# Kernel tuning notes

Measured on AMD Instinct MI355X. Metric: run time of the kernel, lower is better.

Reference implementation:

```python
import jax, jax.numpy as jnp
import numpy as np

EPS = 1e-5
INF = 1e5


def setup_inputs() -> dict:
    key = jax.random.key(0)
    ks = iter(jax.random.split(key, 32))
    B, N, F, H, NH, C = 2, 384, 64, 64, 4, 32
    def lin(k, fi, fo):
        return jax.random.normal(k, (fi, fo), jnp.float32) / np.sqrt(fi).astype(np.float32)
    d = {}
    d['h'] = jax.random.normal(next(ks), (B, N, F), jnp.float32)
    d['x'] = jax.random.normal(next(ks), (B, N, 3), jnp.float32)
    # edge_model (ConcatenationFilter): Linear(2F+1,H), SiLU, Linear(H,H), SiLU
    d['We0'] = lin(next(ks), 2 * F + 1, H); d['be0'] = jnp.zeros(H, jnp.float32)
    d['We1'] = lin(next(ks), H, H);         d['be1'] = jnp.zeros(H, jnp.float32)
    # semantic_attention_mlp: Linear(H, n_heads), LeakyReLU(0.2)
    d['Ws'] = lin(next(ks), H, NH);         d['bs'] = jnp.zeros(NH, jnp.float32)
    # coefficients_mlp: Linear(H,H), SiLU, Linear(H,C)
    d['Wc0'] = lin(next(ks), H, H);         d['bc0'] = jnp.zeros(H, jnp.float32)
    d['Wc1'] = lin(next(ks), H, C);         d['bc1'] = jnp.zeros(C, jnp.float32)
    # post_norm_mlp: Linear(C,H), SiLU, Linear(H,H)
    d['Wp0'] = lin(next(ks), C, H);         d['bp0'] = jnp.zeros(H, jnp.float32)
    d['Wp1'] = lin(next(ks), H, H);         d['bp1'] = jnp.zeros(H, jnp.float32)
    # coordinate_mlp: Linear(H,H), SiLU, Linear(H,1,bias=False) init gain 1e-3
    d['Wx0'] = lin(next(ks), H, H);         d['bx0'] = jnp.zeros(H, jnp.float32)
    d['Wx1'] = lin(next(ks), H, 1) * 1e-3
    # node_mlp: Linear(NH*H + H + F, H), SiLU, Linear(H, F)
    d['Wn0'] = lin(next(ks), NH * H + H + F, H); d['bn0'] = jnp.zeros(H, jnp.float32)
    d['Wn1'] = lin(next(ks), H, F);         d['bn1'] = jnp.zeros(F, jnp.float32)
    d['log_gamma'] = jnp.zeros(NH, jnp.float32)
    return d


def _forward(h, x, We0, be0, We1, be1, Ws, bs, Wc0, bc0, Wc1, bc1,
             Wp0, bp0, Wp1, bp1, Wx0, bx0, Wx1, Wn0, bn0, Wn1, bn1, log_gamma):
    B, N, F = h.shape
    silu = jax.nn.silu

    # pairwise displacements and distances: (B,N,N,3), (B,N,N,1)
    x_minus_xt = x[:, :, None, :] - x[:, None, :, :]
    norm = jnp.sqrt(jnp.sum(x_minus_xt * x_minus_xt, axis=-1, keepdims=True) + EPS)

    # pairwise node-feature concat + distance -> edge MLP (ConcatenationFilter)
    hi = jnp.broadcast_to(h[:, :, None, :], (B, N, N, F))
    hj = jnp.broadcast_to(h[:, None, :, :], (B, N, N, F))
    e_in = jnp.concatenate([hi, hj, norm], axis=-1)           # (B,N,N,2F+1)
    h_e = silu(silu(e_in @ We0 + be0) @ We1 + be1)            # (B,N,N,H)

    eye = jnp.eye(N, dtype=h.dtype)[None, :, :, None]         # mask self-edges

    # euclidean attention per head, softmax over neighbors j (axis=-2)
    eu = jax.nn.softmax(-(norm + INF * eye) * jnp.exp(log_gamma), axis=-2)  # (B,N,N,NH)
    # semantic attention
    sem_logits = jax.nn.leaky_relu(h_e @ Ws + bs, 0.2) - INF * eye
    sem = jax.nn.softmax(sem_logits, axis=-2)                 # (B,N,N,NH)
    comb = eu * sem
    comb = comb / (jnp.sum(comb, axis=-2, keepdims=True) + EPS)

    # attention-weighted multi-head edge features, aggregated over neighbors
    h_e_att = (comb[..., :, None] * h_e[..., None, :]).reshape(B, N, N, -1)  # (B,N,N,NH*H)
    h_e_agg = jnp.sum(h_e_att, axis=-2)                       # (B,N,NH*H)

    # spatial attention: equivariant combinations of unit direction vectors
    coeff = silu(h_e @ Wc0 + bc0) @ Wc1 + bc1                 # (B,N,N,C)
    x_hat = x_minus_xt / (norm + EPS)                         # (B,N,N,3)
    combinations = coeff[..., :, None] * x_hat[..., None, :]  # (B,N,N,C,3)
    comb_sum = jnp.mean(combinations, axis=2)                 # mean over j -> (B,N,C,3)
    comb_norm = jnp.sum(comb_sum * comb_sum, axis=-1)         # (B,N,C)
    h_comb = silu(comb_norm @ Wp0 + bp0) @ Wp1 + bp1          # (B,N,H)

    # node update (residual)
    node_in = jnp.concatenate([h, h_e_agg, h_comb], axis=-1)
    h_out = h + (silu(node_in @ Wn0 + bn0) @ Wn1 + bn1)

    # coordinate update: scalar-gated displacements, mean over neighbors
    scale = silu(h_e @ Wx0 + bx0) @ Wx1                       # (B,N,N,1)
    x_out = x + jnp.mean(x_minus_xt * scale, axis=2)          # (B,N,3)
    return h_out, x_out


def reference(h, x, We0, be0, We1, be1, Ws, bs, Wc0, bc0, Wc1, bc1,
              Wp0, bp0, Wp1, bp1, Wx0, bx0, Wx1, Wn0, bn0, Wn1, bn1, log_gamma):
    return _forward(h, x, We0, be0, We1, be1, Ws, bs, Wc0, bc0, Wc1, bc1,
                    Wp0, bp0, Wp1, bp1, Wx0, bx0, Wx1, Wn0, bn0, Wn1, bn1, log_gamma)
```

## Files before the change

kernel.cpp:

```cpp
#include <hip/hip_runtime.h>

#define NPT 384
#define NB 2
#define HOFF 49152

typedef unsigned short u16;
typedef unsigned int u32;
typedef __bf16 bf16x8 __attribute__((ext_vector_type(8)));
typedef float f32x4 __attribute__((ext_vector_type(4)));

struct alignas(16) U4 { u32 x, y, z, w; };

constexpr float kEPS = 1e-5f;
constexpr float kINF = 1e5f;

__device__ __forceinline__ u16 f2b(float f) {
  u32 x = __float_as_uint(f);
  x += 0x7fffu + ((x >> 16) & 1u);
  return (u16)(x >> 16);
}
__device__ __forceinline__ float b2f(u32 u) { return __uint_as_float(u << 16); }
__device__ __forceinline__ float silu_f(float v) { return v / (1.f + __expf(-v)); }
__device__ __forceinline__ float wredmax(float v) {
#pragma unroll
  for (int m = 32; m >= 1; m >>= 1) v = fmaxf(v, __shfl_xor(v, m, 64));
  return v;
}
__device__ __forceinline__ float wredsum(float v) {
#pragma unroll
  for (int m = 32; m >= 1; m >>= 1) v += __shfl_xor(v, m, 64);
  return v;
}
__device__ __forceinline__ void up8(U4 u, float* f) {
  f[0] = b2f(u.x & 0xffffu); f[1] = b2f(u.x >> 16);
  f[2] = b2f(u.y & 0xffffu); f[3] = b2f(u.y >> 16);
  f[4] = b2f(u.z & 0xffffu); f[5] = b2f(u.z >> 16);
  f[6] = b2f(u.w & 0xffffu); f[7] = b2f(u.w >> 16);
}

__global__ __launch_bounds__(64) void sake_prep(
    const float* __restrict__ h, const float* __restrict__ We0,
    const float* __restrict__ be0, const float* __restrict__ We1,
    const float* __restrict__ Wc0, const float* __restrict__ Wc1,
    const float* __restrict__ Wx0,
    float* __restrict__ U, float* __restrict__ V, u16* __restrict__ WT)
{
  const int t = threadIdx.x;
  const int blk = blockIdx.x;
  if (blk < NB * NPT) {
    __shared__ float hs[64];
    hs[t] = h[blk * 64 + t];
    __syncthreads();
    float u = be0[t], v = 0.f;
#pragma unroll 8
    for (int k = 0; k < 64; k++) {
      float hv = hs[k];
      u = fmaf(hv, We0[k * 64 + t], u);
      v = fmaf(hv, We0[(64 + k) * 64 + t], v);
    }
    U[blk * 64 + t] = u;
    V[blk * 64 + t] = v;
  } else {
    const int wsel = blk - NB * NPT;
    const float* src; int nout; u16* dst;
    if      (wsel == 0) { src = We1; nout = 64; dst = WT;         }
    else if (wsel == 1) { src = Wc0; nout = 64; dst = WT + 4096;  }
    else if (wsel == 2) { src = Wx0; nout = 64; dst = WT + 8192;  }
    else                { src = Wc1; nout = 32; dst = WT + 12288; }
    const int total = 64 * nout;
    for (int o = t; o < total; o += 64) {
      int n = o >> 6, k = o & 63;
      dst[o] = f2b(src[k * nout + n]);
    }
  }
}

struct MainArgs {
  const float *h, *x, *U, *V;
  const u16 *We1T, *Wc0T, *Wx0T, *Wc1T;
  const float *We0, *Ws, *bs, *be1, *bc0, *bc1, *bx0, *Wx1, *log_gamma;
  const float *Wp0, *bp0, *Wp1, *bp1, *Wn0, *bn0, *Wn1, *bn1;
  float* out;
};

__device__ __forceinline__ void gemm64(const u16* aT, const u16* __restrict__ wG,
                                       const float* bias, u16* oT, int w, int lane)
{
  const int m0 = w << 4;
  const int arow = m0 + (lane & 15);
  const int r7 = arow & 7;
  const int kg = lane >> 4;
  bf16x8 a0 = *(const bf16x8*)(aT + arow * 64 + ((kg ^ r7) << 3));
  bf16x8 a1 = *(const bf16x8*)(aT + arow * 64 + ((((kg + 4)) ^ r7) << 3));
#pragma unroll
  for (int nt = 0; nt < 4; nt++) {
    const int col = (nt << 4) + (lane & 15);
    const u16* wrow = wG + col * 64;
    bf16x8 b0 = *(const bf16x8*)(wrow + (kg << 3));
    bf16x8 b1 = *(const bf16x8*)(wrow + 32 + (kg << 3));
    f32x4 acc = {0.f, 0.f, 0.f, 0.f};
    acc = __builtin_amdgcn_mfma_f32_16x16x32_bf16(a0, b0, acc, 0, 0, 0);
    acc = __builtin_amdgcn_mfma_f32_16x16x32_bf16(a1, b1, acc, 0, 0, 0);
    const float bv = bias[col];
    const int cs = col >> 3, ce = col & 7;
#pragma unroll
    for (int r = 0; r < 4; r++) {
      const int row = m0 + (kg << 2) + r;
      oT[row * 64 + ((cs ^ (row & 7)) << 3) + ce] = f2b(silu_f(acc[r] + bv));
    }
  }
}

__global__ __launch_bounds__(256, 3) void sake_main(MainArgs A)
{
  __shared__ __align__(16) u16 buf0[64 * 64];
  __shared__ __align__(16) u16 hes[64 * 64];
  __shared__ __align__(16) u16 coeff[64 * 34];
  __shared__ float WsT[256];
  __shared__ float disp[64][3];
  __shared__ float nrm_s[64];
  __shared__ float sU[64], wd[64], sbe1[64], sbc0[64], sbx0[64], sWx1[64];
  __shared__ float sbc1[32], sbs[4], sgam[4], xi_s[3];
  __shared__ float node_in[384];
  __shared__ float t0s[64];
  __shared__ float cmv[96];

  const int t = threadIdx.x;
  const int w = t >> 6, lane = t & 63;
  const int bi = blockIdx.x;
  const int b = bi / NPT, i = bi - b * NPT;
  const int jj2 = t >> 2, q4 = t & 3;

  if (t < 64) {
    sU[t]   = A.U[bi * 64 + t];
    wd[t]   = A.We0[128 * 64 + t];
    sbe1[t] = A.be1[t];
    sbc0[t] = A.bc0[t];
    sbx0[t] = A.bx0[t];
    sWx1[t] = A.Wx1[t];
    if (t < 32) sbc1[t] = A.bc1[t];
    if (t < 4) { sbs[t] = A.bs[t]; sgam[t] = __expf(A.log_gamma[t]); }
    if (t < 3) xi_s[t] = A.x[(b * NPT + i) * 3 + t];
  }
  WsT[t] = A.Ws[(t & 63) * 4 + (t >> 6)];
  __syncthreads();

  float aReg = 0.f;
  float mL = -1e30f, SL = 0.f, ma = -1e30f, Sa = 0.f, mb = -1e30f, Sb = 0.f;
  float cA0 = 0, cA1 = 0, cA2 = 0, xA0 = 0, xA1 = 0, xA2 = 0;

  for (int jt = 0; jt < 6; ++jt) {
    const int j0 = jt << 6;
    __syncthreads();

    {
      const int j = j0 + jj2;
      const float* xp = &A.x[(b * NPT + j) * 3];
      float dx0 = xi_s[0] - xp[0], dx1 = xi_s[1] - xp[1], dx2 = xi_s[2] - xp[2];
      float nr = sqrtf(fmaf(dx0, dx0, fmaf(dx1, dx1, fmaf(dx2, dx2, kEPS))));
      if (q4 == 0) { disp[jj2][0] = dx0; disp[jj2][1] = dx1; disp[jj2][2] = dx2; nrm_s[jj2] = nr; }
      const float4* vp = (const float4*)(A.V + (size_t)(b * NPT + j) * 64 + q4 * 16);
      float4 v0_ = vp[0], v1_ = vp[1], v2_ = vp[2], v3_ = vp[3];
      float vv[16] = {v0_.x, v0_.y, v0_.z, v0_.w, v1_.x, v1_.y, v1_.z, v1_.w,
                      v2_.x, v2_.y, v2_.z, v2_.w, v3_.x, v3_.y, v3_.z, v3_.w};
      u16 pk[16];
#pragma unroll
      for (int e = 0; e < 16; e++) {
        const int f = q4 * 16 + e;
        pk[e] = f2b(silu_f(sU[f] + vv[e] + nr * wd[f]));
      }
      U4 lo, hi;
      lo.x = pk[0] | ((u32)pk[1] << 16);  lo.y = pk[2] | ((u32)pk[3] << 16);
      lo.z = pk[4] | ((u32)pk[5] << 16);  lo.w = pk[6] | ((u32)pk[7] << 16);
      hi.x = pk[8] | ((u32)pk[9] << 16);  hi.y = pk[10] | ((u32)pk[11] << 16);
      hi.z = pk[12] | ((u32)pk[13] << 16); hi.w = pk[14] | ((u32)pk[15] << 16);
      const int r7 = jj2 & 7;
      *(U4*)(buf0 + jj2 * 64 + (((q4 * 2) ^ r7) << 3)) = lo;
      *(U4*)(buf0 + jj2 * 64 + (((q4 * 2 + 1) ^ r7) << 3)) = hi;
    }
    gemm64(buf0, A.We1T, sbe1, hes, w, lane);
    __syncthreads();

    gemm64(hes, A.Wc0T, sbc0, buf0, w, lane);
    {
      const int m0 = w << 4;
      const int arow = m0 + (lane & 15);
      const int r7a = arow & 7;
      const int kg = lane >> 4;
      bf16x8 a0 = *(const bf16x8*)(buf0 + arow * 64 + ((kg ^ r7a) << 3));
      bf16x8 a1 = *(const bf16x8*)(buf0 + arow * 64 + (((kg + 4) ^ r7a) << 3));
#pragma unroll
      for (int nt = 0; nt < 2; nt++) {
        const int col = (nt << 4) + (lane & 15);
        const u16* wrow = A.Wc1T + col * 64;
        bf16x8 b0 = *(const bf16x8*)(wrow + (kg << 3));
        bf16x8 b1 = *(const bf16x8*)(wrow + 32 + (kg << 3));
        f32x4 acc = {0.f, 0.f, 0.f, 0.f};
        acc = __builtin_amdgcn_mfma_f32_16x16x32_bf16(a0, b0, acc, 0, 0, 0);
        acc = __builtin_amdgcn_mfma_f32_16x16x32_bf16(a1, b1, acc, 0, 0, 0);
        const float bv = sbc1[col];
#pragma unroll
        for (int r = 0; r < 4; r++) {
          const int row = m0 + (kg << 2) + r;
          coeff[row * 34 + col] = f2b(acc[r] + bv);
        }
      }
    }
    {
      const int c = t & 31, g = t >> 5;
#pragma unroll
      for (int it = 0; it < 8; ++it) {
        const int jj = (g << 3) + it;
        const float s = b2f(coeff[jj * 34 + c]) / (nrm_s[jj] + kEPS);
        cA0 = fmaf(s, disp[jj][0], cA0);
        cA1 = fmaf(s, disp[jj][1], cA1);
        cA2 = fmaf(s, disp[jj][2], cA2);
      }
    }
    gemm64(hes, A.Wx0T, sbx0, buf0, w, lane);
    {
      const int jj = jj2;
      const int r7 = jj & 7;
      float acc = 0.f;
#pragma unroll
      for (int c2 = 0; c2 < 2; c2++) {
        const int c = q4 * 2 + c2;
        U4 u = *(const U4*)(buf0 + jj * 64 + ((c ^ r7) << 3));
        float f8[8]; up8(u, f8);
#pragma unroll
        for (int e = 0; e < 8; e++) acc = fmaf(f8[e], sWx1[c * 8 + e], acc);
      }
      acc += __shfl_xor(acc, 1, 64);
      acc += __shfl_xor(acc, 2, 64);
      if (q4 == 0) {
        xA0 = fmaf(disp[jj][0], acc, xA0);
        xA1 = fmaf(disp[jj][1], acc, xA1);
        xA2 = fmaf(disp[jj][2], acc, xA2);
      }
    }
    {
      const int jj = lane, head = w;
      const int r7 = jj & 7;
      float raw = sbs[head];
#pragma unroll
      for (int cc = 0; cc < 8; cc++) {
        U4 u = *(const U4*)(hes + jj * 64 + ((cc ^ r7) << 3));
        float f8[8]; up8(u, f8);
#pragma unroll
        for (int e = 0; e < 8; e++) raw = fmaf(f8[e], WsT[head * 64 + cc * 8 + e], raw);
      }
      float bsem = (raw > 0.f) ? raw : 0.2f * raw;
      const bool self = (j0 + jj) == i;
      if (self) bsem -= kINF;
      const float aeu = -(nrm_s[jj] + (self ? kINF : 0.f)) * sgam[head];
      const float L = aeu + bsem;
      const float nma = fmaxf(ma, wredmax(aeu));
      const float nmb = fmaxf(mb, wredmax(bsem));
      const float nmL = fmaxf(mL, wredmax(L));
      const float eA = __expf(aeu - nma);
      const float eB = __expf(bsem - nmb);
      const float eL = __expf(L - nmL);
      Sa = fmaf(Sa, __expf(ma - nma), wredsum(eA));
      Sb = fmaf(Sb, __expf(mb - nmb), wredsum(eB));
      const float facL = __expf(mL - nmL);
      SL = fmaf(SL, facL, wredsum(eL));
      ma = nma; mb = nmb; mL = nmL;
      aReg *= facL;
      const int fc = lane >> 3, fe = lane & 7;
#pragma unroll 16
      for (int jjj = 0; jjj < 64; jjj++) {
        const float ev = __shfl(eL, jjj, 64);
        aReg = fmaf(ev, b2f(hes[jjj * 64 + ((fc ^ (jjj & 7)) << 3) + fe]), aReg);
      }
    }
  }

  __syncthreads();
  {
    const float Ff = __expf(mL - ma - mb);
    const float denom = fmaf(SL, Ff, kEPS * Sa * Sb);
    node_in[64 + w * 64 + lane] = aReg * (Ff / denom);
  }
  if (t < 64) node_in[t] = A.h[bi * 64 + t];
  float* scratch = (float*)coeff;
  float* xscr = (float*)hes;
  scratch[t * 3 + 0] = cA0; scratch[t * 3 + 1] = cA1; scratch[t * 3 + 2] = cA2;
  if (q4 == 0) { xscr[jj2 * 3 + 0] = xA0; xscr[jj2 * 3 + 1] = xA1; xscr[jj2 * 3 + 2] = xA2; }
  __syncthreads();
  if (t < 96) {
    const int c = t & 31, d = t >> 5;
    float s = 0.f;
#pragma unroll
    for (int g = 0; g < 8; g++) s += scratch[(g * 32 + c) * 3 + d];
    cmv[d * 32 + c] = s * (1.f / 384.f);
  }
  if (t >= 128 && t < 131) {
    const int d = t - 128;
    float s = 0.f;
    for (int k = 0; k < 64; k++) s += xscr[k * 3 + d];
    A.out[HOFF + bi * 3 + d] = xi_s[d] + s * (1.f / 384.f);
  }
  __syncthreads();
  if (t < 32) {
    float v0 = cmv[t], v1 = cmv[32 + t], v2 = cmv[64 + t];
    nrm_s[t] = v0 * v0 + v1 * v1 + v2 * v2;
  }
  __syncthreads();
  if (t < 64) {
    float acc = A.bp0[t];
    for (int c = 0; c < 32; c++) acc = fmaf(nrm_s[c], A.Wp0[c * 64 + t], acc);
    t0s[t] = silu_f(acc);
  }
  __syncthreads();
  if (t < 64) {
    float acc = A.bp1[t];
    for (int k = 0; k < 64; k++) acc = fmaf(t0s[k], A.Wp1[k * 64 + t], acc);
    node_in[320 + t] = acc;
  }
  __syncthreads();
  {
    const int f = t & 63, q = t >> 6;
    float acc = 0.f;
    const int k0 = q * 96;
    for (int k = 0; k < 96; k++) acc = fmaf(node_in[k0 + k], A.Wn0[(k0 + k) * 64 + f], acc);
    scratch[q * 64 + f] = acc;
  }
  __syncthreads();
  if (t < 64) {
    float s = scratch[t] + scratch[64 + t] + scratch[128 + t] + scratch[192 + t] + A.bn0[t];
    t0s[t] = silu_f(s);
  }
  __syncthreads();
  if (t < 64) {
    float acc = A.bn1[t];
    for (int k = 0; k < 64; k++) acc = fmaf(t0s[k], A.Wn1[k * 64 + t], acc);
    A.out[bi * 64 + t] = A.h[bi * 64 + t] + acc;
  }
}

extern "C" void kernel_launch(void* const* d_in, const int* in_sizes, int n_in,
                              void* d_out, int out_size, void* d_ws, size_t ws_size,
                              hipStream_t stream)
{
  (void)in_sizes; (void)n_in; (void)out_size; (void)ws_size;
  const float* h   = (const float*)d_in[0];
  const float* x   = (const float*)d_in[1];
  const float* We0 = (const float*)d_in[2];
  const float* be0 = (const float*)d_in[3];
  const float* We1 = (const float*)d_in[4];
  const float* be1 = (const float*)d_in[5];
  const float* Ws  = (const float*)d_in[6];
  const float* bs  = (const float*)d_in[7];
  const float* Wc0 = (const float*)d_in[8];
  const float* bc0 = (const float*)d_in[9];
  const float* Wc1 = (const float*)d_in[10];
  const float* bc1 = (const float*)d_in[11];
  const float* Wp0 = (const float*)d_in[12];
  const float* bp0 = (const float*)d_in[13];
  const float* Wp1 = (const float*)d_in[14];
  const float* bp1 = (const float*)d_in[15];
  const float* Wx0 = (const float*)d_in[16];
  const float* bx0 = (const float*)d_in[17];
  const float* Wx1 = (const float*)d_in[18];
  const float* Wn0 = (const float*)d_in[19];
  const float* bn0 = (const float*)d_in[20];
  const float* Wn1 = (const float*)d_in[21];
  const float* bn1 = (const float*)d_in[22];
  const float* lg  = (const float*)d_in[23];

  float* U = (float*)d_ws;
  float* V = U + NB * NPT * 64;
  u16* WT = (u16*)(V + NB * NPT * 64);

  sake_prep<<<NB * NPT + 4, 64, 0, stream>>>(h, We0, be0, We1, Wc0, Wc1, Wx0, U, V, WT);

  MainArgs A;
  A.h = h; A.x = x; A.U = U; A.V = V;
  A.We1T = WT; A.Wc0T = WT + 4096; A.Wx0T = WT + 8192; A.Wc1T = WT + 12288;
  A.We0 = We0; A.Ws = Ws; A.bs = bs; A.be1 = be1; A.bc0 = bc0; A.bc1 = bc1;
  A.bx0 = bx0; A.Wx1 = Wx1; A.log_gamma = lg;
  A.Wp0 = Wp0; A.bp0 = bp0; A.Wp1 = Wp1; A.bp1 = bp1;
  A.Wn0 = Wn0; A.bn0 = bn0; A.Wn1 = Wn1; A.bn1 = bn1;
  A.out = (float*)d_out;

  sake_main<<<NB * NPT, 256, 0, stream>>>(A);
}
```

Before: 111.7 us.

## Move semantic attention logits and attention aggregation onto MFMA

Computes the per-head semantic attention logits with an MFMA against a padded bf16 copy of Ws, replacing the scalar dot-product loop. The attention-weighted aggregation over neighbors, which used a shuffle-based scalar loop, becomes an MFMA between the bf16 exponent matrix and a transposed copy of h_e that the first GEMM now also writes. It also drops the running max for the distance softmax by summing exp(aeu) directly, and swaps a divide for a precomputed reciprocal norm. The cost is extra LDS buffers, two more block barriers per tile, and bf16 rounding of the softmax weights.

```diff
diff --git a/kernel.cpp b/kernel.cpp
--- a/kernel.cpp
+++ b/kernel.cpp
@@ -42,7 +42,7 @@
     const float* __restrict__ h, const float* __restrict__ We0,
     const float* __restrict__ be0, const float* __restrict__ We1,
     const float* __restrict__ Wc0, const float* __restrict__ Wc1,
-    const float* __restrict__ Wx0,
+    const float* __restrict__ Wx0, const float* __restrict__ Ws,
     float* __restrict__ U, float* __restrict__ V, u16* __restrict__ WT)
 {
   const int t = threadIdx.x;
@@ -62,6 +62,14 @@
     V[blk * 64 + t] = v;
   } else {
     const int wsel = blk - NB * NPT;
+    if (wsel == 4) {
+      u16* dst = WT + 14336;
+      for (int o = t; o < 16 * 64; o += 64) {
+        int c = o >> 6, k = o & 63;
+        dst[o] = (c < 4) ? f2b(Ws[k * 4 + c]) : (u16)0;
+      }
+      return;
+    }
     const float* src; int nout; u16* dst;
     if      (wsel == 0) { src = We1; nout = 64; dst = WT;         }
     else if (wsel == 1) { src = Wc0; nout = 64; dst = WT + 4096;  }
@@ -77,14 +85,15 @@
 
 struct MainArgs {
   const float *h, *x, *U, *V;
-  const u16 *We1T, *Wc0T, *Wx0T, *Wc1T;
-  const float *We0, *Ws, *bs, *be1, *bc0, *bc1, *bx0, *Wx1, *log_gamma;
+  const u16 *We1T, *Wc0T, *Wx0T, *Wc1T, *WsPT;
+  const float *We0, *bs, *be1, *bc0, *bc1, *bx0, *Wx1, *log_gamma;
   const float *Wp0, *bp0, *Wp1, *bp1, *Wn0, *bn0, *Wn1, *bn1;
   float* out;
 };
 
+template<bool DUALT>
 __device__ __forceinline__ void gemm64(const u16* aT, const u16* __restrict__ wG,
-                                       const float* bias, u16* oT, int w, int lane)
+                                       const float* bias, u16* oT, u16* oTT, int w, int lane)
 {
   const int m0 = w << 4;
   const int arow = m0 + (lane & 15);
@@ -106,7 +115,10 @@
 #pragma unroll
     for (int r = 0; r < 4; r++) {
       const int row = m0 + (kg << 2) + r;
-      oT[row * 64 + ((cs ^ (row & 7)) << 3) + ce] = f2b(silu_f(acc[r] + bv));
+      const u16 v = f2b(silu_f(acc[r] + bv));
+      oT[row * 64 + ((cs ^ (row & 7)) << 3) + ce] = v;
+      if constexpr (DUALT)
+        oTT[col * 64 + ((((row >> 3)) ^ (col & 7)) << 3) + (row & 7)] = v;
     }
   }
 }
@@ -115,12 +127,16 @@
 {
   __shared__ __align__(16) u16 buf0[64 * 64];
   __shared__ __align__(16) u16 hes[64 * 64];
+  __shared__ __align__(16) u16 hesT[64 * 64];
+  __shared__ __align__(16) u16 E_lds[16 * 64];
   __shared__ __align__(16) u16 coeff[64 * 34];
-  __shared__ float WsT[256];
+  __shared__ float raw_lds[64 * 5];
   __shared__ float disp[64][3];
   __shared__ float nrm_s[64];
+  __shared__ float invn_s[64];
   __shared__ float sU[64], wd[64], sbe1[64], sbc0[64], sbx0[64], sWx1[64];
   __shared__ float sbc1[32], sbs[4], sgam[4], xi_s[3];
+  __shared__ float facL_s[4], coefh_s[4];
   __shared__ float node_in[384];
   __shared__ float t0s[64];
   __shared__ float cmv[96];
@@ -142,11 +158,11 @@
     if (t < 4) { sbs[t] = A.bs[t]; sgam[t] = __expf(A.log_gamma[t]); }
     if (t < 3) xi_s[t] = A.x[(b * NPT + i) * 3 + t];
   }
-  WsT[t] = A.Ws[(t & 63) * 4 + (t >> 6)];
-  __syncthreads();
-
-  float aReg = 0.f;
-  float mL = -1e30f, SL = 0.f, ma = -1e30f, Sa = 0.f, mb = -1e30f, Sb = 0.f;
+  ((u32*)E_lds)[t] = 0; ((u32*)E_lds)[256 + t] = 0;
+  __syncthreads();
+
+  f32x4 aFrag = {0.f, 0.f, 0.f, 0.f};
+  float mL = -1e30f, SL = 0.f, mb = -1e30f, Sb = 0.f, saPart = 0.f;
   float cA0 = 0, cA1 = 0, cA2 = 0, xA0 = 0, xA1 = 0, xA2 = 0;
 
   for (int jt = 0; jt < 6; ++jt) {
@@ -158,7 +174,10 @@
       const float* xp = &A.x[(b * NPT + j) * 3];
       float dx0 = xi_s[0] - xp[0], dx1 = xi_s[1] - xp[1], dx2 = xi_s[2] - xp[2];
       float nr = sqrtf(fmaf(dx0, dx0, fmaf(dx1, dx1, fmaf(dx2, dx2, kEPS))));
-      if (q4 == 0) { disp[jj2][0] = dx0; disp[jj2][1] = dx1; disp[jj2][2] = dx2; nrm_s[jj2] = nr; }
+      if (q4 == 0) {
+        disp[jj2][0] = dx0; disp[jj2][1] = dx1; disp[jj2][2] = dx2;
+        nrm_s[jj2] = nr; invn_s[jj2] = 1.f / (nr + kEPS);
+      }
       const float4* vp = (const float4*)(A.V + (size_t)(b * NPT + j) * 64 + q4 * 16);
       float4 v0_ = vp[0], v1_ = vp[1], v2_ = vp[2], v3_ = vp[3];
       float vv[16] = {v0_.x, v0_.y, v0_.z, v0_.w, v1_.x, v1_.y, v1_.z, v1_.w,
@@ -178,10 +197,10 @@
       *(U4*)(buf0 + jj2 * 64 + (((q4 * 2) ^ r7) << 3)) = lo;
       *(U4*)(buf0 + jj2 * 64 + (((q4 * 2 + 1) ^ r7) << 3)) = hi;
     }
-    gemm64(buf0, A.We1T, sbe1, hes, w, lane);
+    gemm64<true>(buf0, A.We1T, sbe1, hes, hesT, w, lane);
     __syncthreads();
 
-    gemm64(hes, A.Wc0T, sbc0, buf0, w, lane);
+    gemm64<false>(hes, A.Wc0T, sbc0, buf0, nullptr, w, lane);
     {
       const int m0 = w << 4;
       const int arow = m0 + (lane & 15);
@@ -211,13 +230,13 @@
 #pragma unroll
       for (int it = 0; it < 8; ++it) {
         const int jj = (g << 3) + it;
-        const float s = b2f(coeff[jj * 34 + c]) / (nrm_s[jj] + kEPS);
+        const float s = b2f(coeff[jj * 34 + c]) * invn_s[jj];
         cA0 = fmaf(s, disp[jj][0], cA0);
         cA1 = fmaf(s, disp[jj][1], cA1);
         cA2 = fmaf(s, disp[jj][2], cA2);
       }
     }
-    gemm64(hes, A.Wx0T, sbx0, buf0, w, lane);
+    gemm64<false>(hes, A.Wx0T, sbx0, buf0, nullptr, w, lane);
     {
       const int jj = jj2;
       const int r7 = jj & 7;
@@ -239,54 +258,85 @@
       }
     }
     {
+      const int m0 = w << 4;
+      const int arow = m0 + (lane & 15);
+      const int r7a = arow & 7;
+      const int kg = lane >> 4;
+      bf16x8 a0 = *(const bf16x8*)(hes + arow * 64 + ((kg ^ r7a) << 3));
+      bf16x8 a1 = *(const bf16x8*)(hes + arow * 64 + (((kg + 4) ^ r7a) << 3));
+      const u16* wrow = A.WsPT + (lane & 15) * 64;
+      bf16x8 b0 = *(const bf16x8*)(wrow + (kg << 3));
+      bf16x8 b1 = *(const bf16x8*)(wrow + 32 + (kg << 3));
+      f32x4 acc = {0.f, 0.f, 0.f, 0.f};
+      acc = __builtin_amdgcn_mfma_f32_16x16x32_bf16(a0, b0, acc, 0, 0, 0);
+      acc = __builtin_amdgcn_mfma_f32_16x16x32_bf16(a1, b1, acc, 0, 0, 0);
+      if ((lane & 15) < 4) {
+#pragma unroll
+        for (int r = 0; r < 4; r++)
+          raw_lds[(m0 + (kg << 2) + r) * 5 + (lane & 15)] = acc[r];
+      }
+    }
+    __syncthreads();
+
+    {
       const int jj = lane, head = w;
-      const int r7 = jj & 7;
-      float raw = sbs[head];
-#pragma unroll
-      for (int cc = 0; cc < 8; cc++) {
-        U4 u = *(const U4*)(hes + jj * 64 + ((cc ^ r7) << 3));
-        float f8[8]; up8(u, f8);
-#pragma unroll
-        for (int e = 0; e < 8; e++) raw = fmaf(f8[e], WsT[head * 64 + cc * 8 + e], raw);
-      }
+      float raw = raw_lds[jj * 5 + head] + sbs[head];
       float bsem = (raw > 0.f) ? raw : 0.2f * raw;
       const bool self = (j0 + jj) == i;
       if (self) bsem -= kINF;
       const float aeu = -(nrm_s[jj] + (self ? kINF : 0.f)) * sgam[head];
       const float L = aeu + bsem;
-      const float nma = fmaxf(ma, wredmax(aeu));
       const float nmb = fmaxf(mb, wredmax(bsem));
       const float nmL = fmaxf(mL, wredmax(L));
-      const float eA = __expf(aeu - nma);
+      saPart += __expf(aeu);
       const float eB = __expf(bsem - nmb);
       const float eL = __expf(L - nmL);
-      Sa = fmaf(Sa, __expf(ma - nma), wredsum(eA));
       Sb = fmaf(Sb, __expf(mb - nmb), wredsum(eB));
       const float facL = __expf(mL - nmL);
       SL = fmaf(SL, facL, wredsum(eL));
-      ma = nma; mb = nmb; mL = nmL;
-      aReg *= facL;
-      const int fc = lane >> 3, fe = lane & 7;
-#pragma unroll 16
-      for (int jjj = 0; jjj < 64; jjj++) {
-        const float ev = __shfl(eL, jjj, 64);
-        aReg = fmaf(ev, b2f(hes[jjj * 64 + ((fc ^ (jjj & 7)) << 3) + fe]), aReg);
-      }
-    }
-  }
-
-  __syncthreads();
-  {
-    const float Ff = __expf(mL - ma - mb);
-    const float denom = fmaf(SL, Ff, kEPS * Sa * Sb);
-    node_in[64 + w * 64 + lane] = aReg * (Ff / denom);
-  }
-  if (t < 64) node_in[t] = A.h[bi * 64 + t];
+      mb = nmb; mL = nmL;
+      E_lds[head * 64 + (((jj >> 3) ^ head) << 3) + (jj & 7)] = f2b(eL);
+      if (lane == 0) facL_s[head] = facL;
+    }
+    __syncthreads();
+
+    {
+      const int kg = lane >> 4;
+      const int erow = lane & 15;
+      const int e7 = erow & 7;
+      bf16x8 ea0 = *(const bf16x8*)(E_lds + erow * 64 + ((kg ^ e7) << 3));
+      bf16x8 ea1 = *(const bf16x8*)(E_lds + erow * 64 + (((kg + 4) ^ e7) << 3));
+      const int f = (w << 4) + (lane & 15);
+      const int f7 = f & 7;
+      bf16x8 hb0 = *(const bf16x8*)(hesT + f * 64 + ((kg ^ f7) << 3));
+      bf16x8 hb1 = *(const bf16x8*)(hesT + f * 64 + (((kg + 4) ^ f7) << 3));
+#pragma unroll
+      for (int r = 0; r < 4; r++) aFrag[r] *= facL_s[r];
+      aFrag = __builtin_amdgcn_mfma_f32_16x16x32_bf16(ea0, hb0, aFrag, 0, 0, 0);
+      aFrag = __builtin_amdgcn_mfma_f32_16x16x32_bf16(ea1, hb1, aFrag, 0, 0, 0);
+    }
+  }
+
+  __syncthreads();
   float* scratch = (float*)coeff;
   float* xscr = (float*)hes;
   scratch[t * 3 + 0] = cA0; scratch[t * 3 + 1] = cA1; scratch[t * 3 + 2] = cA2;
   if (q4 == 0) { xscr[jj2 * 3 + 0] = xA0; xscr[jj2 * 3 + 1] = xA1; xscr[jj2 * 3 + 2] = xA2; }
-  __syncthreads();
+  {
+    const float Sa = wredsum(saPart);
+    if (lane == 0) {
+      const float Ff = __expf(mL - mb);
+      const float denom = fmaf(SL, Ff, kEPS * Sa * Sb);
+      coefh_s[w] = Ff / denom;
+    }
+  }
+  if (t < 64) node_in[t] = A.h[bi * 64 + t];
+  __syncthreads();
+  if (lane < 16) {
+#pragma unroll
+    for (int r = 0; r < 4; r++)
+      node_in[64 + r * 64 + (w << 4) + lane] = aFrag[r] * coefh_s[r];
+  }
   if (t < 96) {
     const int c = t & 31, d = t >> 5;
     float s = 0.f;
@@ -372,12 +422,13 @@
   float* V = U + NB * NPT * 64;
   u16* WT = (u16*)(V + NB * NPT * 64);
 
-  sake_prep<<<NB * NPT + 4, 64, 0, stream>>>(h, We0, be0, We1, Wc0, Wc1, Wx0, U, V, WT);
+  sake_prep<<<NB * NPT + 5, 64, 0, stream>>>(h, We0, be0, We1, Wc0, Wc1, Wx0, Ws, U, V, WT);
 
   MainArgs A;
   A.h = h; A.x = x; A.U = U; A.V = V;
   A.We1T = WT; A.Wc0T = WT + 4096; A.Wx0T = WT + 8192; A.Wc1T = WT + 12288;
-  A.We0 = We0; A.Ws = Ws; A.bs = bs; A.be1 = be1; A.bc0 = bc0; A.bc1 = bc1;
+  A.WsPT = WT + 14336;
+  A.We0 = We0; A.bs = bs; A.be1 = be1; A.bc0 = bc0; A.bc1 = bc1;
   A.bx0 = bx0; A.Wx1 = Wx1; A.log_gamma = lg;
   A.Wp0 = Wp0; A.bp0 = bp0; A.Wp1 = Wp1; A.bp1 = bp1;
   A.Wn0 = Wn0; A.bn0 = bn0; A.Wn1 = Wn1; A.bn1 = bn1;
```

New measurement: 118.6 us. 1.06x slower.
